# Kernel tuning notes

Measured on AMD Instinct MI355X. Metric: run time of the kernel, lower is better.

The kernel has to match this reference:

```python
import jax, jax.numpy as jnp
import numpy as np

B, H, S, D = 2, 16, 2048, 64

def setup_inputs() -> dict:
    key = jax.random.key(0)
    kq, kk, kv, km, ks = jax.random.split(key, 5)
    return {
        "query_input": jax.random.normal(kq, (B, H, S, D), dtype=jnp.float32),
        "key_input": jax.random.normal(kk, (B, H, S, D), dtype=jnp.float32),
        "value_input": jax.random.normal(kv, (B, H, S, D), dtype=jnp.float32),
        "query_mask": jnp.ones((B, 1, S, 1), dtype=jnp.float32),
        "key_mask": jax.random.uniform(km, (B, 1, 1, S), dtype=jnp.float32),
        "scale_factor": jax.random.normal(ks, (B, 1, 1, 1), dtype=jnp.float32),
        "dropout": 0,
    }

def reference(query_input, key_input, value_input, query_mask, key_mask, scale_factor, dropout):
    # qk = q @ k^T  -> [B, H, S, S]
    qk = jnp.einsum("bhqd,bhkd->bhqk", query_input, key_input)
    scaled_qk = qk * scale_factor                      # elementwise per-batch scale
    softmax_qk = jax.nn.softmax(scaled_qk, axis=-1)
    masked = softmax_qk * key_mask                     # post-softmax multiplicative mask
    # dropout with p=0 is the identity (deterministic baseline)
    output = jnp.einsum("bhqk,bhkd->bhqd", masked, value_input)
    return output
```

## Files before the change

### kernel.cpp

```cpp
#include <hip/hip_runtime.h>
#include <hip/hip_bf16.h>
#include <stdint.h>

#define BB 2
#define HH 16
#define SS 2048
#define DD 64
constexpr int BH = BB * HH;
constexpr int NT = SS / 64;

typedef _Float16 f16_t;
typedef f16_t f16x8 __attribute__((ext_vector_type(8)));
typedef float f32x4 __attribute__((ext_vector_type(4)));

__device__ __forceinline__ uint32_t pkf16(float a, float b) {
    return __builtin_bit_cast(uint32_t, __builtin_amdgcn_cvt_pkrtz(a, b));
}

__global__ __launch_bounds__(256)
void fattn5(const float* __restrict__ Qg, const float* __restrict__ Kg,
            const float* __restrict__ Vg, const float* __restrict__ Mg,
            const float* __restrict__ Sg, float* __restrict__ Og)
{
    __shared__ __align__(16) f16_t Kh_lds[64][72];
    __shared__ __align__(16) f16_t Vt_lds[64][72];
    __shared__ __align__(16) f16_t Pt_lds[4][16][72];
    __shared__ float msk_lds[SS];

    const int bh   = blockIdx.x % BH;
    const int qt   = blockIdx.x / BH;
    const int b    = bh / HH;
    const int tid  = threadIdx.x;
    const int wave = tid >> 6;
    const int lane = tid & 63;
    const int l16  = lane & 15;
    const int quad = lane >> 4;

    const float sc = Sg[b] * 1.44269504088896340736f;
    const size_t base = (size_t)bh * SS * DD;
    const int q0 = qt * 64 + wave * 16;

    for (int i = tid; i < SS; i += 256) msk_lds[i] = Mg[(size_t)b * SS + i];

    f16x8 qf[2];
    {
        const float* qp = Qg + base + (size_t)(q0 + l16) * DD + quad * 8;
#pragma unroll
        for (int kc = 0; kc < 2; ++kc) {
            float4 a  = *(const float4*)(qp + kc * 32);
            float4 b4 = *(const float4*)(qp + kc * 32 + 4);
            f16x8 f;
            f[0] = (f16_t)(a.x * sc);  f[1] = (f16_t)(a.y * sc);
            f[2] = (f16_t)(a.z * sc);  f[3] = (f16_t)(a.w * sc);
            f[4] = (f16_t)(b4.x * sc); f[5] = (f16_t)(b4.y * sc);
            f[6] = (f16_t)(b4.z * sc); f[7] = (f16_t)(b4.w * sc);
            qf[kc] = f;
        }
    }

    f32x4 Ot[4];
#pragma unroll
    for (int mt = 0; mt < 4; ++mt) Ot[mt] = f32x4{0.f, 0.f, 0.f, 0.f};
    float m_run = -1e30f, l_run = 0.0f;

    const int krow = tid >> 2;
    const int kcol = (tid & 3) * 16;
    const int vd   = tid & 63;
    const int vk0  = wave * 16;

    for (int kt = 0; kt < NT; ++kt) {
        __syncthreads();

        {
            const float* kp = Kg + base + (size_t)(kt * 64 + krow) * DD + kcol;
            float4 a0 = *(const float4*)(kp);
            float4 a1 = *(const float4*)(kp + 4);
            float4 a2 = *(const float4*)(kp + 8);
            float4 a3 = *(const float4*)(kp + 12);
            uint4 w0 = make_uint4(pkf16(a0.x, a0.y), pkf16(a0.z, a0.w),
                                  pkf16(a1.x, a1.y), pkf16(a1.z, a1.w));
            uint4 w1 = make_uint4(pkf16(a2.x, a2.y), pkf16(a2.z, a2.w),
                                  pkf16(a3.x, a3.y), pkf16(a3.z, a3.w));
            *(uint4*)&Kh_lds[krow][kcol]     = w0;
            *(uint4*)&Kh_lds[krow][kcol + 8] = w1;
        }
        {
            const float* vp = Vg + base + (size_t)(kt * 64 + vk0) * DD + vd;
            const float* mp = &msk_lds[kt * 64 + vk0];
#pragma unroll
            for (int j = 0; j < 4; ++j) {
                float v0 = vp[(4 * j + 0) * DD] * mp[4 * j + 0];
                float v1 = vp[(4 * j + 1) * DD] * mp[4 * j + 1];
                float v2 = vp[(4 * j + 2) * DD] * mp[4 * j + 2];
                float v3 = vp[(4 * j + 3) * DD] * mp[4 * j + 3];
                uint2 w = make_uint2(pkf16(v0, v1), pkf16(v2, v3));
                *(uint2*)&Vt_lds[vd][vk0 + 4 * j] = w;
            }
        }
        __syncthreads();

        f32x4 Sfr[4];
#pragma unroll
        for (int mt = 0; mt < 4; ++mt) {
            f32x4 acc = f32x4{0.f, 0.f, 0.f, 0.f};
#pragma unroll
            for (int kc = 0; kc < 2; ++kc) {
                f16x8 kh = *(const f16x8*)&Kh_lds[mt * 16 + l16][kc * 32 + quad * 8];
                acc = __builtin_amdgcn_mfma_f32_16x16x32_f16(kh, qf[kc], acc, 0, 0, 0);
            }
            Sfr[mt] = acc;
        }

        float mx = Sfr[0][0];
#pragma unroll
        for (int mt = 0; mt < 4; ++mt)
#pragma unroll
            for (int r = 0; r < 4; ++r) mx = fmaxf(mx, Sfr[mt][r]);
        mx = fmaxf(mx, __shfl_xor(mx, 16));
        mx = fmaxf(mx, __shfl_xor(mx, 32));

        if (__any(mx > m_run)) {
            const float mnew  = fmaxf(m_run, mx);
            const float alpha = exp2f(m_run - mnew);
            m_run = mnew;
            l_run *= alpha;
#pragma unroll
            for (int mt = 0; mt < 4; ++mt) Ot[mt] *= alpha;
        }

        float ps[4][4];
        float rs = 0.0f;
#pragma unroll
        for (int mt = 0; mt < 4; ++mt)
#pragma unroll
            for (int r = 0; r < 4; ++r) {
                ps[mt][r] = exp2f(Sfr[mt][r] - m_run);
                rs += ps[mt][r];
            }
        rs += __shfl_xor(rs, 16);
        rs += __shfl_xor(rs, 32);
        l_run += rs;

#pragma unroll
        for (int mt = 0; mt < 4; ++mt) {
            uint2 w = make_uint2(pkf16(ps[mt][0], ps[mt][1]),
                                 pkf16(ps[mt][2], ps[mt][3]));
            *(uint2*)&Pt_lds[wave][l16][mt * 16 + quad * 4] = w;
        }

#pragma unroll
        for (int kc = 0; kc < 2; ++kc) {
            f16x8 pf = *(const f16x8*)&Pt_lds[wave][l16][kc * 32 + quad * 8];
#pragma unroll
            for (int mt = 0; mt < 4; ++mt) {
                f16x8 vf = *(const f16x8*)&Vt_lds[mt * 16 + l16][kc * 32 + quad * 8];
                Ot[mt] = __builtin_amdgcn_mfma_f32_16x16x32_f16(vf, pf, Ot[mt], 0, 0, 0);
            }
        }
    }

    const float inv = 1.0f / l_run;
    float* op = Og + base + (size_t)(q0 + l16) * DD + quad * 4;
#pragma unroll
    for (int mt = 0; mt < 4; ++mt) {
#pragma unroll
        for (int r = 0; r < 4; ++r)
            op[mt * 16 + r] = Ot[mt][r] * inv;
    }
}

extern "C" void kernel_launch(void* const* d_in, const int* in_sizes, int n_in,
                              void* d_out, int out_size, void* d_ws, size_t ws_size,
                              hipStream_t stream) {
    const float* Qg = (const float*)d_in[0];
    const float* Kg = (const float*)d_in[1];
    const float* Vg = (const float*)d_in[2];
    const float* Mg = (const float*)d_in[4];
    const float* Sg = (const float*)d_in[5];
    float* Og = (float*)d_out;

    fattn5<<<dim3(BH * NT), dim3(256), 0, stream>>>(Qg, Kg, Vg, Mg, Sg, Og);
}
```

Baseline: 180.2 us.

## Double query tile per block to 128 rows with 512 threads sharing K/V tiles

Each block now covers 128 query rows using 8 waves instead of 64 rows with 4 waves, and the grid is halved. Every K/V tile staged in shared memory serves twice as many queries, which halves global K/V reads and fp16 conversion work per query. The cooperative K and V load patterns are re-split so each of the 512 threads converts a smaller piece. The trade-off is 512 blocks, about two per CU on a 256-CU part, so occupancy and latency hiding may drop.

```diff
diff --git a/kernel.cpp b/kernel.cpp
--- a/kernel.cpp
+++ b/kernel.cpp
@@ -8,6 +8,7 @@
 #define DD 64
 constexpr int BH = BB * HH;
 constexpr int NT = SS / 64;
+constexpr int QB = 16;
 
 typedef _Float16 f16_t;
 typedef f16_t f16x8 __attribute__((ext_vector_type(8)));
@@ -17,14 +18,14 @@
     return __builtin_bit_cast(uint32_t, __builtin_amdgcn_cvt_pkrtz(a, b));
 }
 
-__global__ __launch_bounds__(256)
-void fattn5(const float* __restrict__ Qg, const float* __restrict__ Kg,
+__global__ __launch_bounds__(512)
+void fattn6(const float* __restrict__ Qg, const float* __restrict__ Kg,
             const float* __restrict__ Vg, const float* __restrict__ Mg,
             const float* __restrict__ Sg, float* __restrict__ Og)
 {
     __shared__ __align__(16) f16_t Kh_lds[64][72];
     __shared__ __align__(16) f16_t Vt_lds[64][72];
-    __shared__ __align__(16) f16_t Pt_lds[4][16][72];
+    __shared__ __align__(16) f16_t Pt_lds[8][16][72];
     __shared__ float msk_lds[SS];
 
     const int bh   = blockIdx.x % BH;
@@ -38,9 +39,9 @@
 
     const float sc = Sg[b] * 1.44269504088896340736f;
     const size_t base = (size_t)bh * SS * DD;
-    const int q0 = qt * 64 + wave * 16;
+    const int q0 = qt * 128 + wave * 16;
 
-    for (int i = tid; i < SS; i += 256) msk_lds[i] = Mg[(size_t)b * SS + i];
+    for (int i = tid; i < SS; i += 512) msk_lds[i] = Mg[(size_t)b * SS + i];
 
     f16x8 qf[2];
     {
@@ -63,39 +64,32 @@
     for (int mt = 0; mt < 4; ++mt) Ot[mt] = f32x4{0.f, 0.f, 0.f, 0.f};
     float m_run = -1e30f, l_run = 0.0f;
 
-    const int krow = tid >> 2;
-    const int kcol = (tid & 3) * 16;
+    const int krow = tid >> 3;
+    const int kc8  = (tid & 7) * 8;
     const int vd   = tid & 63;
-    const int vk0  = wave * 16;
+    const int vk0  = (tid >> 6) * 8;
 
     for (int kt = 0; kt < NT; ++kt) {
         __syncthreads();
 
         {
-            const float* kp = Kg + base + (size_t)(kt * 64 + krow) * DD + kcol;
+            const float* kp = Kg + base + (size_t)(kt * 64 + krow) * DD + kc8;
             float4 a0 = *(const float4*)(kp);
             float4 a1 = *(const float4*)(kp + 4);
-            float4 a2 = *(const float4*)(kp + 8);
-            float4 a3 = *(const float4*)(kp + 12);
-            uint4 w0 = make_uint4(pkf16(a0.x, a0.y), pkf16(a0.z, a0.w),
-                                  pkf16(a1.x, a1.y), pkf16(a1.z, a1.w));
-            uint4 w1 = make_uint4(pkf16(a2.x, a2.y), pkf16(a2.z, a2.w),
-                                  pkf16(a3.x, a3.y), pkf16(a3.z, a3.w));
-            *(uint4*)&Kh_lds[krow][kcol]     = w0;
-            *(uint4*)&Kh_lds[krow][kcol + 8] = w1;
+            uint4 w = make_uint4(pkf16(a0.x, a0.y), pkf16(a0.z, a0.w),
+                                 pkf16(a1.x, a1.y), pkf16(a1.z, a1.w));
+            *(uint4*)&Kh_lds[krow][kc8] = w;
         }
         {
             const float* vp = Vg + base + (size_t)(kt * 64 + vk0) * DD + vd;
             const float* mp = &msk_lds[kt * 64 + vk0];
-#pragma unroll
-            for (int j = 0; j < 4; ++j) {
-                float v0 = vp[(4 * j + 0) * DD] * mp[4 * j + 0];
-                float v1 = vp[(4 * j + 1) * DD] * mp[4 * j + 1];
-                float v2 = vp[(4 * j + 2) * DD] * mp[4 * j + 2];
-                float v3 = vp[(4 * j + 3) * DD] * mp[4 * j + 3];
-                uint2 w = make_uint2(pkf16(v0, v1), pkf16(v2, v3));
-                *(uint2*)&Vt_lds[vd][vk0 + 4 * j] = w;
-            }
+            float v0 = vp[0 * DD] * mp[0], v1 = vp[1 * DD] * mp[1];
+            float v2 = vp[2 * DD] * mp[2], v3 = vp[3 * DD] * mp[3];
+            float v4 = vp[4 * DD] * mp[4], v5 = vp[5 * DD] * mp[5];
+            float v6 = vp[6 * DD] * mp[6], v7 = vp[7 * DD] * mp[7];
+            uint4 w = make_uint4(pkf16(v0, v1), pkf16(v2, v3),
+                                 pkf16(v4, v5), pkf16(v6, v7));
+            *(uint4*)&Vt_lds[vd][vk0] = w;
         }
         __syncthreads();
 
@@ -179,5 +173,5 @@
     const float* Sg = (const float*)d_in[5];
     float* Og = (float*)d_out;
 
-    fattn5<<<dim3(BH * NT), dim3(256), 0, stream>>>(Qg, Kg, Vg, Mg, Sg, Og);
+    fattn6<<<dim3(BH * QB), dim3(512), 0, stream>>>(Qg, Kg, Vg, Mg, Sg, Og);
 }
```

New measurement: 169.0 us. 1.07x faster.
